# Performance work log

Measured on AMD Instinct MI355X. Metric: run time of the kernel, lower is better.

## Reference

```python
import jax, jax.numpy as jnp
import numpy as np

PADDING_VALUE = 0.0  # padding_value init arg


def setup_inputs() -> dict:
    key = jax.random.key(0)
    k1, k2 = jax.random.split(key)
    B, T, D = 16, 4096, 256
    x = jax.random.normal(k1, (B, T, D), dtype=jnp.float32)
    mask = jax.random.bernoulli(k2, 0.5, (B, T))  # bool
    return {"x": x, "mask": mask}


def reference(x, mask):
    # batch_first=True: x is [B, T, ...feat], mask is [B, T].
    B, T = mask.shape
    lens = mask.sum(axis=1)  # [B] number of selected elements per row
    # Stable argsort on (~mask) brings indices of True entries to the front,
    # preserving their original order -> index of the j-th True element.
    order = jnp.argsort(jnp.logical_not(mask), axis=1, stable=True)  # [B, T]
    # Gather x rows into compacted order.
    idx = order.reshape(order.shape + (1,) * (x.ndim - 2))  # [B, T, 1...]
    gathered = jnp.take_along_axis(x, idx, axis=1)  # [B, T, ...feat]
    # Right-pad positions j >= lens[b] with padding_value.
    valid = jnp.arange(T)[None, :] < lens[:, None]  # [B, T]
    valid = valid.reshape(valid.shape + (1,) * (x.ndim - 2))
    x_ = jnp.where(valid, gathered, jnp.asarray(PADDING_VALUE, x.dtype))
    return x_, lens
```

## Files before the change

kernel.cpp:

```cpp
#include <hip/hip_runtime.h>


#define BLK 256
#define NW (BLK / 64)
#define ROWS 64

__global__ __launch_bounds__(BLK) void pad_masked_fused(
    const float* __restrict__ x,
    const int* __restrict__ mask,
    float* __restrict__ out,
    float* __restrict__ lens_f,
    int T, int D4) {

    const int c = blockIdx.x;
    const int b = blockIdx.y;
    const int tid = threadIdx.x;
    const int lane = tid & 63;
    const int wave = tid >> 6;
    const int j0 = c * ROWS;

    const int* mrow = mask + (size_t)b * T;

    int pre = 0, all = 0;
    for (int e = tid * 4; e < T; e += BLK * 4) {
        const int4 mv = *reinterpret_cast<const int4*>(mrow + e);
        const int t0 = (mv.x != 0), t1 = (mv.y != 0), t2 = (mv.z != 0), t3 = (mv.w != 0);
        all += t0 + t1 + t2 + t3;
        if (e + 3 < j0) {
            pre += t0 + t1 + t2 + t3;
        } else if (e < j0) {
            pre += t0;
            pre += (e + 1 < j0) ? t1 : 0;
            pre += (e + 2 < j0) ? t2 : 0;
            pre += (e + 3 < j0) ? t3 : 0;
        }
    }
    unsigned long long packed =
        (unsigned long long)pre | ((unsigned long long)all << 32);
    #pragma unroll
    for (int off = 32; off; off >>= 1) packed += __shfl_xor(packed, off);

    __shared__ unsigned long long wred[NW];
    __shared__ int selRows[ROWS];
    __shared__ int nsel;
    if (lane == 0) wred[wave] = packed;
    __syncthreads();

    unsigned long long tot = 0;
    #pragma unroll
    for (int w = 0; w < NW; ++w) tot += wred[w];
    const int P = (int)(tot & 0xffffffffull);
    const int L = (int)(tot >> 32);

    if (wave == 0) {
        const int m = (mrow[j0 + lane] != 0);
        int incl = m;
        #pragma unroll
        for (int off = 1; off < 64; off <<= 1) {
            const int v = __shfl_up(incl, off);
            if (lane >= off) incl += v;
        }
        if (m) selRows[incl - 1] = lane;
        if (lane == 63) nsel = incl;
    }
    __syncthreads();
    const int n = nsel;

    if (c == 0 && tid == 0) lens_f[b] = (float)L;

    const float4* xrow = reinterpret_cast<const float4*>(x) +
                         ((size_t)b * T + j0) * (size_t)D4;
    float4* obase = reinterpret_cast<float4*>(out) + (size_t)b * T * (size_t)D4;
    const float4 z = make_float4(0.f, 0.f, 0.f, 0.f);

    for (int i = wave; i < n; i += 2 * NW) {
        const int i2 = i + NW;
        const bool h2 = (i2 < n);
        const int r0 = selRows[i];
        const int r1 = h2 ? selRows[i2] : 0;
        for (int t = lane; t < D4; t += 64) {
            const float4 v0 = xrow[(size_t)r0 * D4 + t];
            float4 v1 = z;
            if (h2) v1 = xrow[(size_t)r1 * D4 + t];
            obase[(size_t)(P + i) * D4 + t] = v0;
            if (h2) obase[(size_t)(P + i2) * D4 + t] = v1;
        }
    }

    const int zstart = (L > j0) ? L : j0;
    for (int j = zstart + wave; j < j0 + ROWS; j += NW) {
        for (int t = lane; t < D4; t += 64)
            obase[(size_t)j * D4 + t] = z;
    }
}

extern "C" void kernel_launch(void* const* d_in, const int* in_sizes, int n_in,
                              void* d_out, int out_size, void* d_ws, size_t ws_size,
                              hipStream_t stream) {
    const float* x = (const float*)d_in[0];
    const int* mask = (const int*)d_in[1];

    const int Nx = in_sizes[0];
    const int BT = in_sizes[1];
    const int B = out_size - Nx;
    const int T = BT / B;
    const int D = Nx / BT;
    const int D4 = D / 4;

    float* out = (float*)d_out;
    float* lens_f = out + (size_t)Nx;

    dim3 grid(T / ROWS, B);
    pad_masked_fused<<<grid, BLK, 0, stream>>>(x, mask, out, lens_f, T, D4);
}
```

Baseline: 22.61 us.

## Use single-wave blocks with ballot-based row compaction and nontemporal stores

Switches to one 64-lane wave per block handling 16 rows, so the cross-wave LDS reduction, the shared selected-row list and both __syncthreads go away. Selected rows come from a ballot bitmask walked with ctz instead of a shuffle prefix scan. Output writes use nontemporal stores to avoid polluting cache. Each block now rereads the full mask row to compute its prefix, and blocks are 4x more numerous, so redundant mask traffic grows considerably. The prefix simplification (e < j0 whole-int4) stays correct because j0 is a multiple of 16.

```diff
diff --git a/kernel.cpp b/kernel.cpp
--- a/kernel.cpp
+++ b/kernel.cpp
@@ -1,9 +1,10 @@
 #include <hip/hip_runtime.h>
 
 
-#define BLK 256
-#define NW (BLK / 64)
-#define ROWS 64
+typedef float f32x4 __attribute__((ext_vector_type(4)));
+
+#define BLK 64
+#define ROWS 16
 
 __global__ __launch_bounds__(BLK) void pad_masked_fused(
     const float* __restrict__ x,
@@ -14,84 +15,55 @@
 
     const int c = blockIdx.x;
     const int b = blockIdx.y;
-    const int tid = threadIdx.x;
-    const int lane = tid & 63;
-    const int wave = tid >> 6;
+    const int lane = threadIdx.x;
     const int j0 = c * ROWS;
 
     const int* mrow = mask + (size_t)b * T;
 
     int pre = 0, all = 0;
-    for (int e = tid * 4; e < T; e += BLK * 4) {
+    for (int e = lane * 4; e < T; e += BLK * 4) {
         const int4 mv = *reinterpret_cast<const int4*>(mrow + e);
-        const int t0 = (mv.x != 0), t1 = (mv.y != 0), t2 = (mv.z != 0), t3 = (mv.w != 0);
-        all += t0 + t1 + t2 + t3;
-        if (e + 3 < j0) {
-            pre += t0 + t1 + t2 + t3;
-        } else if (e < j0) {
-            pre += t0;
-            pre += (e + 1 < j0) ? t1 : 0;
-            pre += (e + 2 < j0) ? t2 : 0;
-            pre += (e + 3 < j0) ? t3 : 0;
-        }
+        const int s4 = (mv.x != 0) + (mv.y != 0) + (mv.z != 0) + (mv.w != 0);
+        all += s4;
+        if (e < j0) pre += s4;
     }
-    unsigned long long packed =
-        (unsigned long long)pre | ((unsigned long long)all << 32);
+    unsigned long long packed = (unsigned long long)(unsigned)pre |
+                                ((unsigned long long)(unsigned)all << 32);
     #pragma unroll
     for (int off = 32; off; off >>= 1) packed += __shfl_xor(packed, off);
+    const int P = (int)(packed & 0xffffffffull);
+    const int L = (int)(packed >> 32);
 
-    __shared__ unsigned long long wred[NW];
-    __shared__ int selRows[ROWS];
-    __shared__ int nsel;
-    if (lane == 0) wred[wave] = packed;
-    __syncthreads();
+    if (c == 0 && lane == 0) lens_f[b] = (float)L;
 
-    unsigned long long tot = 0;
-    #pragma unroll
-    for (int w = 0; w < NW; ++w) tot += wred[w];
-    const int P = (int)(tot & 0xffffffffull);
-    const int L = (int)(tot >> 32);
+    const int myrow = (lane < ROWS) ? (mrow[j0 + lane] != 0) : 0;
+    unsigned long long s = __ballot(myrow);
 
-    if (wave == 0) {
-        const int m = (mrow[j0 + lane] != 0);
-        int incl = m;
-        #pragma unroll
-        for (int off = 1; off < 64; off <<= 1) {
-            const int v = __shfl_up(incl, off);
-            if (lane >= off) incl += v;
+    const f32x4* xrow = reinterpret_cast<const f32x4*>(x) +
+                        ((size_t)b * T + j0) * (size_t)D4;
+    f32x4* obase = reinterpret_cast<f32x4*>(out) + (size_t)b * T * (size_t)D4;
+    const f32x4 z = {0.f, 0.f, 0.f, 0.f};
+
+    int i = 0;
+    while (s) {
+        const int r0 = (int)__builtin_ctzll(s); s &= s - 1;
+        const bool h2 = (s != 0);
+        const int r1 = h2 ? (int)__builtin_ctzll(s) : 0;
+        if (h2) s &= s - 1;
+        for (int t = lane; t < D4; t += 64) {
+            const f32x4 v0 = xrow[(size_t)r0 * D4 + t];
+            f32x4 v1 = z;
+            if (h2) v1 = xrow[(size_t)r1 * D4 + t];
+            __builtin_nontemporal_store(v0, &obase[(size_t)(P + i) * D4 + t]);
+            if (h2) __builtin_nontemporal_store(v1, &obase[(size_t)(P + i + 1) * D4 + t]);
         }
-        if (m) selRows[incl - 1] = lane;
-        if (lane == 63) nsel = incl;
-    }
-    __syncthreads();
-    const int n = nsel;
-
-    if (c == 0 && tid == 0) lens_f[b] = (float)L;
-
-    const float4* xrow = reinterpret_cast<const float4*>(x) +
-                         ((size_t)b * T + j0) * (size_t)D4;
-    float4* obase = reinterpret_cast<float4*>(out) + (size_t)b * T * (size_t)D4;
-    const float4 z = make_float4(0.f, 0.f, 0.f, 0.f);
-
-    for (int i = wave; i < n; i += 2 * NW) {
-        const int i2 = i + NW;
-        const bool h2 = (i2 < n);
-        const int r0 = selRows[i];
-        const int r1 = h2 ? selRows[i2] : 0;
-        for (int t = lane; t < D4; t += 64) {
-            const float4 v0 = xrow[(size_t)r0 * D4 + t];
-            float4 v1 = z;
-            if (h2) v1 = xrow[(size_t)r1 * D4 + t];
-            obase[(size_t)(P + i) * D4 + t] = v0;
-            if (h2) obase[(size_t)(P + i2) * D4 + t] = v1;
-        }
+        i += h2 ? 2 : 1;
     }
 
     const int zstart = (L > j0) ? L : j0;
-    for (int j = zstart + wave; j < j0 + ROWS; j += NW) {
+    for (int j = zstart; j < j0 + ROWS; ++j)
         for (int t = lane; t < D4; t += 64)
-            obase[(size_t)j * D4 + t] = z;
-    }
+            __builtin_nontemporal_store(z, &obase[(size_t)j * D4 + t]);
 }
 
 extern "C" void kernel_launch(void* const* d_in, const int* in_sizes, int n_in,
```

After: 24.72 us. +9.3%, slower.
